# Kernel tuning notes

Measured on AMD Instinct MI355X. Metric: run time of the kernel, lower is better.

## Reference

```python
import jax, jax.numpy as jnp
import numpy as np

D_MODEL = 512
N_HEADS = 8


def setup_inputs() -> dict:
    key = jax.random.key(0)
    ks = jax.random.split(key, 16)
    bs, S, D = 16, 512, D_MODEL
    def lin(k, fo, fi):
        lim = np.sqrt(6.0 / (fi + fo)).astype(np.float32)
        return jax.random.uniform(k, (fo, fi), jnp.float32, -lim, lim)
    inp = {
        'q': jax.random.normal(ks[0], (bs, S, D), jnp.float32),
        'k': jax.random.normal(ks[1], (bs, S, D), jnp.float32),
        'v': jax.random.normal(ks[2], (bs, S, D), jnp.float32),
        'sgap': jax.random.randint(ks[3], (bs, S), 0, 100, jnp.int64) if jax.config.jax_enable_x64 else jax.random.randint(ks[3], (bs, S), 0, 100, jnp.int32),
        'pcount': jax.random.randint(ks[4], (bs, S), 0, 50, jnp.int32),
        'Wq': lin(ks[5], D, D), 'bq': jnp.zeros((D,), jnp.float32),
        'Wk': lin(ks[6], D, D), 'bk': jnp.zeros((D,), jnp.float32),
        'Wv': lin(ks[7], D, D), 'bv': jnp.zeros((D,), jnp.float32),
        'Wo': lin(ks[8], D, D), 'bo': jnp.zeros((D,), jnp.float32),
        'gammas': jax.random.normal(ks[9], (N_HEADS, 1, 1), jnp.float32) * 0.5,
        'ln_g': jnp.ones((D,), jnp.float32), 'ln_b': jnp.zeros((D,), jnp.float32),
        'Wi1': lin(ks[10], D // 4, 2), 'bi1': jnp.zeros((D // 4,), jnp.float32),
        'Wi2': lin(ks[11], D, D // 4), 'bi2': jnp.zeros((D,), jnp.float32),
        'iscale': jnp.array([0.5], jnp.float32),
    }
    return inp


def reference(q, k, v, sgap, pcount, Wq, bq, Wk, bk, Wv, bv, Wo, bo, gammas, ln_g, ln_b, Wi1, bi1, Wi2, bi2, iscale):
    bs, S, D = q.shape
    h = gammas.shape[0]
    d_k = D // h
    def split_heads(x, W, b):
        return (x @ W.T + b).reshape(bs, S, h, d_k).transpose(0, 2, 1, 3)  # [b,h,S,d]
    qh = split_heads(q, Wq, bq)
    kh = split_heads(k, Wk, bk)
    vh = split_heads(v, Wv, bv)

    scores = jnp.einsum('bhid,bhjd->bhij', qh, kh) / jnp.sqrt(jnp.float32(d_k))
    # strict-causal mask (triu(ones,k=0)==0): attend only to j < i
    mask = jnp.tril(jnp.ones((S, S), bool), k=-1)[None, None]
    NEG = jnp.float32(-1e32)

    # no-grad temporal distance term
    p = jax.nn.softmax(jnp.where(mask, scores, NEG), axis=-1) * mask
    distcum = jnp.cumsum(p, axis=-1)
    disttotal = jnp.sum(p, axis=-1, keepdims=True)
    idx = jnp.arange(S, dtype=jnp.float32)
    pos = jnp.abs(idx[None, :] - idx[:, None])[None, None]
    dist = jax.lax.stop_gradient(jnp.sqrt(jnp.clip((disttotal - distcum) * pos, 0.0, None)))

    gam = -jax.nn.softplus(gammas)[None]  # [1,h,1,1]
    temporal = jnp.clip(jnp.exp(dist * gam), 1e-5, 1e5)
    attn = jax.nn.softmax(jnp.where(mask, scores * temporal, NEG), axis=-1)
    attn = attn.at[:, :, 0, :].set(0.0)  # zero_pad first query position

    X = jnp.einsum('bhij,bhjd->bhid', attn, vh).transpose(0, 2, 1, 3).reshape(bs, S, D)

    # InterferenceAddNorm
    def norm01(x):
        x = x.astype(jnp.float32)
        std = jnp.std(x, ddof=1) + 1e-6
        return (jnp.tanh((x - jnp.mean(x)) / std) + 1.0) / 2.0
    ii = jnp.stack([norm01(sgap), norm01(pcount)], axis=-1)  # [b,S,2]
    feat = jax.nn.relu(ii @ Wi1.T + bi1) @ Wi2.T + bi2
    Y = X + iscale * feat
    mu = jnp.mean(Y, -1, keepdims=True)
    var = jnp.var(Y, -1, keepdims=True)
    Yn = (Y - mu) / jnp.sqrt(var + 1e-5) * ln_g + ln_b
    return Yn @ Wo.T + bo
```

## Files before the change

### kernel.cpp

```cpp
#include <hip/hip_runtime.h>
#include <hip/hip_bf16.h>
#include <math.h>

typedef __attribute__((ext_vector_type(8))) short bf16x8;
typedef __attribute__((ext_vector_type(4))) float f32x4;
typedef __fp16 __attribute__((ext_vector_type(2))) h16x2;

__device__ __forceinline__ f32x4 mfma16(bf16x8 a, bf16x8 b, f32x4 c) {
  return __builtin_amdgcn_mfma_f32_16x16x32_bf16(a, b, c, 0, 0, 0);
}

__device__ __forceinline__ float scan16(float x) {
  int v;
  v = __builtin_amdgcn_update_dpp(0, __float_as_int(x), 0x111, 0xf, 0xf, true);
  x += __int_as_float(v);
  v = __builtin_amdgcn_update_dpp(0, __float_as_int(x), 0x112, 0xf, 0xf, true);
  x += __int_as_float(v);
  v = __builtin_amdgcn_update_dpp(0, __float_as_int(x), 0x114, 0xf, 0xf, true);
  x += __int_as_float(v);
  v = __builtin_amdgcn_update_dpp(0, __float_as_int(x), 0x118, 0xf, 0xf, true);
  x += __int_as_float(v);
  return x;
}

__global__ void stats_kernel(const int* __restrict__ sgap,
                             const int* __restrict__ pcount,
                             float* __restrict__ stats) {
  const int N = 16 * 512;
  long long s0 = 0, q0 = 0, s1 = 0, q1 = 0;
  for (int i = threadIdx.x; i < N; i += 256) {
    long long a = sgap[i];
    long long b = pcount[i];
    s0 += a; q0 += a * a;
    s1 += b; q1 += b * b;
  }
#pragma unroll
  for (int m = 32; m >= 1; m >>= 1) {
    s0 += __shfl_xor(s0, m, 64); q0 += __shfl_xor(q0, m, 64);
    s1 += __shfl_xor(s1, m, 64); q1 += __shfl_xor(q1, m, 64);
  }
  __shared__ long long red[4][4];
  const int w = threadIdx.x >> 6;
  if ((threadIdx.x & 63) == 0) {
    red[w][0] = s0; red[w][1] = q0; red[w][2] = s1; red[w][3] = q1;
  }
  __syncthreads();
  if (threadIdx.x == 0) {
    long long S0 = 0, Q0 = 0, S1 = 0, Q1 = 0;
    for (int i = 0; i < 4; ++i) {
      S0 += red[i][0]; Q0 += red[i][1]; S1 += red[i][2]; Q1 += red[i][3];
    }
    const double n = (double)N;
    const double mean0 = S0 / n, mean1 = S1 / n;
    const double var0 = ((double)Q0 - (double)S0 * (double)S0 / n) / (n - 1.0);
    const double var1 = ((double)Q1 - (double)S1 * (double)S1 / n) / (n - 1.0);
    const float std0 = (float)sqrt(var0) + 1e-6f;
    const float std1 = (float)sqrt(var1) + 1e-6f;
    stats[0] = (float)mean0; stats[1] = 1.0f / std0;
    stats[2] = (float)mean1; stats[3] = 1.0f / std1;
  }
}

template <int AMODE>
__device__ __forceinline__ void gemm_body(const void* __restrict__ Ain,
                                          const float* __restrict__ W,
                                          const float* __restrict__ bias,
                                          void* __restrict__ Out, const int omode) {
  constexpr int LDK = 40;
  __shared__ __hip_bfloat16 As[128 * LDK];
  __shared__ __hip_bfloat16 Bs[64 * LDK];
  const int tid = threadIdx.x;
  const int tm = blockIdx.x * 128;
  const int tn = blockIdx.y * 64;
  const int lane = tid & 63;
  const int wid = tid >> 6;
  const int wm = wid * 32;
  const int g = lane >> 4, l15 = lane & 15;

  const f32x4 Z = {0.f, 0.f, 0.f, 0.f};
  f32x4 acc[2][4];
#pragma unroll
  for (int m = 0; m < 2; ++m)
#pragma unroll
    for (int n = 0; n < 4; ++n) acc[m][n] = Z;

  for (int k0 = 0; k0 < 512; k0 += 32) {
#pragma unroll
    for (int p = 0; p < 4; ++p) {
      const int c = p * 256 + tid;
      const int row = c >> 3;
      const int kc = (c & 7) * 4;
      union { __hip_bfloat16 h[4]; uint2 u; } ua;
      if (AMODE == 0) {
        const float4 x = *(const float4*)((const float*)Ain + (size_t)(tm + row) * 512 + k0 + kc);
        ua.h[0] = __float2bfloat16(x.x); ua.h[1] = __float2bfloat16(x.y);
        ua.h[2] = __float2bfloat16(x.z); ua.h[3] = __float2bfloat16(x.w);
      } else {
        ua.u = *(const uint2*)((const __hip_bfloat16*)Ain + (size_t)(tm + row) * 512 + k0 + kc);
      }
      *(uint2*)&As[row * LDK + kc] = ua.u;
      if (p < 2) {
        union { __hip_bfloat16 h[4]; uint2 u; } ub;
        const float4 wv = *(const float4*)(W + (size_t)(tn + row) * 512 + k0 + kc);
        ub.h[0] = __float2bfloat16(wv.x); ub.h[1] = __float2bfloat16(wv.y);
        ub.h[2] = __float2bfloat16(wv.z); ub.h[3] = __float2bfloat16(wv.w);
        *(uint2*)&Bs[row * LDK + kc] = ub.u;
      }
    }
    __syncthreads();
    bf16x8 af[2], bfv[4];
#pragma unroll
    for (int m = 0; m < 2; ++m)
      af[m] = *(const bf16x8*)&As[(wm + m * 16 + l15) * LDK + g * 8];
#pragma unroll
    for (int n = 0; n < 4; ++n)
      bfv[n] = *(const bf16x8*)&Bs[(n * 16 + l15) * LDK + g * 8];
#pragma unroll
    for (int m = 0; m < 2; ++m)
#pragma unroll
      for (int n = 0; n < 4; ++n)
        acc[m][n] = mfma16(af[m], bfv[n], acc[m][n]);
    __syncthreads();
  }

#pragma unroll
  for (int n = 0; n < 4; ++n) {
    const int cc = tn + n * 16 + l15;
    const float bv = bias[cc];
#pragma unroll
    for (int m = 0; m < 2; ++m) {
#pragma unroll
      for (int jj = 0; jj < 4; ++jj) {
        const int r = tm + wm + m * 16 + g * 4 + jj;
        const float v = acc[m][n][jj] + bv;
        if (omode == 2) {
          ((float*)Out)[(size_t)r * 512 + cc] = v;
        } else {
          const int bb = r >> 9, srow = r & 511, hh = cc >> 6, dd = cc & 63;
          if (omode == 0)
            ((__hip_bfloat16*)Out)[(((size_t)(bb * 8 + hh)) * 512 + srow) * 64 + dd] =
                __float2bfloat16(v);
          else
            ((__hip_bfloat16*)Out)[(((size_t)(bb * 8 + hh)) * 64 + dd) * 512 + srow] =
                __float2bfloat16(v);
        }
      }
    }
  }
}

__global__ __launch_bounds__(256) void gemm_qkv(
    const float* __restrict__ q, const float* __restrict__ k,
    const float* __restrict__ v, const float* __restrict__ Wq,
    const float* __restrict__ bq, const float* __restrict__ Wk,
    const float* __restrict__ bk, const float* __restrict__ Wv,
    const float* __restrict__ bv, __hip_bfloat16* __restrict__ qh,
    __hip_bfloat16* __restrict__ kh, __hip_bfloat16* __restrict__ vhT) {
  const int z = blockIdx.z;
  const float* A = (z == 0) ? q : (z == 1) ? k : v;
  const float* W = (z == 0) ? Wq : (z == 1) ? Wk : Wv;
  const float* bias = (z == 0) ? bq : (z == 1) ? bk : bv;
  void* Out = (z == 0) ? (void*)qh : (z == 1) ? (void*)kh : (void*)vhT;
  gemm_body<0>(A, W, bias, Out, (z == 2) ? 1 : 0);
}

__global__ __launch_bounds__(256) void gemm_wo(const __hip_bfloat16* __restrict__ Yn,
                                               const float* __restrict__ Wo,
                                               const float* __restrict__ bo,
                                               float* __restrict__ Out) {
  gemm_body<1>(Yn, Wo, bo, Out, 2);
}

#define PLD 40

__device__ __forceinline__ void attn_unit(
    const __hip_bfloat16* __restrict__ Q, const __hip_bfloat16* __restrict__ K,
    const __hip_bfloat16* __restrict__ V, __hip_bfloat16* __restrict__ Xb,
    __hip_bfloat16* Pw, const int i0, const int ntile, const float gam,
    const int b, const int h, const int lane) {
  const int g = lane >> 4, l15 = lane & 15;
  const float scale = 0.125f;
  const f32x4 Z = {0.f, 0.f, 0.f, 0.f};

  const bf16x8 qf0 = *(const bf16x8*)&Q[(i0 + l15) * 64 + g * 8];
  const bf16x8 qf1 = *(const bf16x8*)&Q[(i0 + l15) * 64 + 32 + g * 8];

  h16x2 sp[64];
  float d1p[4] = {0.f, 0.f, 0.f, 0.f};
#pragma unroll
  for (int t = 0; t < 32; ++t) {
    if (t < ntile) {
      const bf16x8 kf0 = *(const bf16x8*)&K[(t * 16 + l15) * 64 + g * 8];
      const bf16x8 kf1 = *(const bf16x8*)&K[(t * 16 + l15) * 64 + 32 + g * 8];
      f32x4 s = mfma16(qf0, kf0, Z);
      s = mfma16(qf1, kf1, s);
      sp[2 * t] = __builtin_amdgcn_cvt_pkrtz(s[0] * scale, s[1] * scale);
      sp[2 * t + 1] = __builtin_amdgcn_cvt_pkrtz(s[2] * scale, s[3] * scale);
      const int j = t * 16 + l15;
#pragma unroll
      for (int jj = 0; jj < 4; ++jj) {
        const float sv = (float)((jj < 2) ? sp[2 * t][jj] : sp[2 * t + 1][jj - 2]);
        const int i = i0 + g * 4 + jj;
        d1p[jj] += (j < i) ? __expf(sv) : 0.f;
      }
    }
  }
  float invd1[4];
#pragma unroll
  for (int jj = 0; jj < 4; ++jj) {
    float dd = d1p[jj];
#pragma unroll
    for (int m = 8; m >= 1; m >>= 1) dd += __shfl_xor(dd, m, 16);
    invd1[jj] = dd > 0.f ? 1.f / dd : 0.f;
  }

  f32x4 accx[4] = {Z, Z, Z, Z};
  float carry[4] = {0.f, 0.f, 0.f, 0.f};
  float d2p[4] = {0.f, 0.f, 0.f, 0.f};

#pragma unroll
  for (int tp = 0; tp < 16; ++tp) {
    if (tp * 2 < ntile) {
      __hip_bfloat16* Pb = Pw + (tp & 1) * (16 * PLD);
#pragma unroll
      for (int half = 0; half < 2; ++half) {
        const int t = tp * 2 + half;
        float e2v[4] = {0.f, 0.f, 0.f, 0.f};
        if (t < ntile) {
          const int j = t * 16 + l15;
#pragma unroll
          for (int jj = 0; jj < 4; ++jj) {
            const float sv = (float)((jj < 2) ? sp[2 * t][jj] : sp[2 * t + 1][jj - 2]);
            const int i = i0 + g * 4 + jj;
            const bool valid = j < i;
            const float p = valid ? __expf(sv) * invd1[jj] : 0.f;
            const float cs = scan16(p) + carry[jj];
            const float suffix = 1.f - cs;
            carry[jj] = __shfl(cs, 15, 16);
            const float dist = sqrtf(fmaxf(suffix * (float)(i - j), 0.f));
            const float tempo = fmaxf(__expf(gam * dist), 1e-5f);
            const float e2 = valid ? __expf(sv * tempo) : 0.f;
            d2p[jj] += e2;
            e2v[jj] = e2;
          }
        }
#pragma unroll
        for (int jj = 0; jj < 4; ++jj)
          Pb[(g * 4 + jj) * PLD + half * 16 + l15] = __float2bfloat16(e2v[jj]);
      }
      asm volatile("s_waitcnt lgkmcnt(0)" ::: "memory");
      const bf16x8 pf = *(const bf16x8*)&Pb[l15 * PLD + g * 8];
#pragma unroll
      for (int n = 0; n < 4; ++n) {
        const bf16x8 vf =
            *(const bf16x8*)&V[(size_t)(n * 16 + l15) * 512 + tp * 32 + g * 8];
        accx[n] = mfma16(pf, vf, accx[n]);
      }
    }
  }

#pragma unroll
  for (int jj = 0; jj < 4; ++jj) {
    float dd = d2p[jj];
#pragma unroll
    for (int m = 8; m >= 1; m >>= 1) dd += __shfl_xor(dd, m, 16);
    d2p[jj] = dd > 0.f ? 1.f / dd : 0.f;
  }
#pragma unroll
  for (int n = 0; n < 4; ++n) {
#pragma unroll
    for (int jj = 0; jj < 4; ++jj) {
      const int i = i0 + g * 4 + jj;
      const float val = (i > 0) ? accx[n][jj] * d2p[jj] : 0.f;
      Xb[((size_t)(b * 512 + i)) * 512 + h * 64 + n * 16 + l15] = __float2bfloat16(val);
    }
  }
}

__global__ __launch_bounds__(64, 4) void attn_kernel(
    const __hip_bfloat16* __restrict__ qh, const __hip_bfloat16* __restrict__ kh,
    const __hip_bfloat16* __restrict__ vhT, const float* __restrict__ gammas,
    __hip_bfloat16* __restrict__ Xb) {
  __shared__ __hip_bfloat16 Psh[2 * 16 * PLD];
  const int lane = threadIdx.x;
  const int work = (blockIdx.x & 7) * 512 + (blockIdx.x >> 3);
  const int bh = work >> 5;
  const int rg = work & 31;
  const int b = bh >> 3, h = bh & 7;

  const __hip_bfloat16* Q = qh + (size_t)bh * (512 * 64);
  const __hip_bfloat16* K = kh + (size_t)bh * (512 * 64);
  const __hip_bfloat16* V = vhT + (size_t)bh * (64 * 512);
  const float gam = -log1pf(expf(gammas[h]));

  attn_unit(Q, K, V, Xb, Psh, rg * 16, rg + 1, gam, b, h, lane);
}

__global__ __launch_bounds__(256) void addnorm_kernel(
    const __hip_bfloat16* __restrict__ Xb, const int* __restrict__ sgap,
    const int* __restrict__ pcount, const float* __restrict__ stats,
    const float* __restrict__ Wi1, const float* __restrict__ bi1,
    const float* __restrict__ Wi2, const float* __restrict__ bi2,
    const float* __restrict__ iscale, const float* __restrict__ ln_g,
    const float* __restrict__ ln_b, __hip_bfloat16* __restrict__ Yn) {
  constexpr int WLD = 132;
  __shared__ __hip_bfloat16 Hs[16 * WLD];
  __shared__ float iis[16][2];
  __shared__ float red[4][16][2];
  const int tid = threadIdx.x;
  const int lane = tid & 63;
  const int w = tid >> 6;
  const int g = lane >> 4, l15 = lane & 15;
  const int t0 = blockIdx.x * 16;

  if (tid < 16) {
    const float a0 = ((float)sgap[t0 + tid] - stats[0]) * stats[1];
    const float a1 = ((float)pcount[t0 + tid] - stats[2]) * stats[3];
    iis[tid][0] = (tanhf(a0) + 1.f) * 0.5f;
    iis[tid][1] = (tanhf(a1) + 1.f) * 0.5f;
  }
  __syncthreads();

  {
    const int tt = tid & 15;
    const int jb = (tid >> 4) * 8;
    const float a = iis[tt][0], b = iis[tt][1];
#pragma unroll
    for (int jj = 0; jj < 8; ++jj) {
      const int j = jb + jj;
      const float hv = fmaxf(Wi1[j * 2] * a + Wi1[j * 2 + 1] * b + bi1[j], 0.f);
      Hs[tt * WLD + j] = __float2bfloat16(hv);
    }
  }
  __syncthreads();

  const f32x4 Z = {0.f, 0.f, 0.f, 0.f};
  f32x4 acc[8];
#pragma unroll
  for (int n = 0; n < 8; ++n) acc[n] = Z;

#pragma unroll
  for (int k = 0; k < 4; ++k) {
    const bf16x8 af = *(const bf16x8*)&Hs[l15 * WLD + k * 32 + g * 8];
#pragma unroll
    for (int n = 0; n < 8; ++n) {
      const int col = w * 128 + n * 16 + l15;
      const float4 x0 = *(const float4*)(Wi2 + (size_t)col * 128 + k * 32 + g * 8);
      const float4 x1 = *(const float4*)(Wi2 + (size_t)col * 128 + k * 32 + g * 8 + 4);
      union { __hip_bfloat16 hh[8]; bf16x8 v8; } ub;
      ub.hh[0] = __float2bfloat16(x0.x); ub.hh[1] = __float2bfloat16(x0.y);
      ub.hh[2] = __float2bfloat16(x0.z); ub.hh[3] = __float2bfloat16(x0.w);
      ub.hh[4] = __float2bfloat16(x1.x); ub.hh[5] = __float2bfloat16(x1.y);
      ub.hh[6] = __float2bfloat16(x1.z); ub.hh[7] = __float2bfloat16(x1.w);
      acc[n] = mfma16(af, ub.v8, acc[n]);
    }
  }

  const float sc = iscale[0];
  float bi[8], lg[8], lb[8];
#pragma unroll
  for (int nn = 0; nn < 8; ++nn) {
    const int c = w * 128 + nn * 16 + l15;
    bi[nn] = bi2[c]; lg[nn] = ln_g[c]; lb[nn] = ln_b[c];
  }

#pragma unroll
  for (int jj = 0; jj < 4; ++jj) {
    const int r = g * 4 + jj;
    float s = 0.f, sq = 0.f;
#pragma unroll
    for (int nn = 0; nn < 8; ++nn) {
      const int c = w * 128 + nn * 16 + l15;
      const float fv = acc[nn][jj] + bi[nn];
      const float y = __bfloat162float(Xb[(size_t)(t0 + r) * 512 + c]) + sc * fv;
      acc[nn][jj] = y;
      s += y; sq += y * y;
    }
#pragma unroll
    for (int mk = 8; mk >= 1; mk >>= 1) {
      s += __shfl_xor(s, mk, 16);
      sq += __shfl_xor(sq, mk, 16);
    }
    if (l15 == 0) { red[w][r][0] = s; red[w][r][1] = sq; }
  }
  __syncthreads();

#pragma unroll
  for (int jj = 0; jj < 4; ++jj) {
    const int r = g * 4 + jj;
    const float sum = red[0][r][0] + red[1][r][0] + red[2][r][0] + red[3][r][0];
    const float sqs = red[0][r][1] + red[1][r][1] + red[2][r][1] + red[3][r][1];
    const float mu = sum * (1.f / 512.f);
    const float var = sqs * (1.f / 512.f) - mu * mu;
    const float rstd = rsqrtf(var + 1e-5f);
#pragma unroll
    for (int nn = 0; nn < 8; ++nn) {
      const int c = w * 128 + nn * 16 + l15;
      Yn[(size_t)(t0 + r) * 512 + c] =
          __float2bfloat16((acc[nn][jj] - mu) * rstd * lg[nn] + lb[nn]);
    }
  }
}

extern "C" void kernel_launch(void* const* d_in, const int* in_sizes, int n_in,
                              void* d_out, int out_size, void* d_ws, size_t ws_size,
                              hipStream_t stream) {
  const float* q = (const float*)d_in[0];
  const float* k = (const float*)d_in[1];
  const float* v = (const float*)d_in[2];
  const int* sgap = (const int*)d_in[3];
  const int* pcount = (const int*)d_in[4];
  const float* Wq = (const float*)d_in[5];
  const float* bq = (const float*)d_in[6];
  const float* Wk = (const float*)d_in[7];
  const float* bk = (const float*)d_in[8];
  const float* Wv = (const float*)d_in[9];
  const float* bv = (const float*)d_in[10];
  const float* Wo = (const float*)d_in[11];
  const float* bo = (const float*)d_in[12];
  const float* gammas = (const float*)d_in[13];
  const float* ln_g = (const float*)d_in[14];
  const float* ln_b = (const float*)d_in[15];
  const float* Wi1 = (const float*)d_in[16];
  const float* bi1 = (const float*)d_in[17];
  const float* Wi2 = (const float*)d_in[18];
  const float* bi2 = (const float*)d_in[19];
  const float* iscale = (const float*)d_in[20];

  char* ws = (char*)d_ws;
  __hip_bfloat16* qh = (__hip_bfloat16*)(ws);
  __hip_bfloat16* kh = (__hip_bfloat16*)(ws + ((size_t)8 << 20));
  __hip_bfloat16* vhT = (__hip_bfloat16*)(ws + ((size_t)16 << 20));
  __hip_bfloat16* Xb = (__hip_bfloat16*)(ws + ((size_t)24 << 20));
  __hip_bfloat16* Yn = (__hip_bfloat16*)(ws + ((size_t)32 << 20));
  float* stats = (float*)(ws + ((size_t)40 << 20));

  stats_kernel<<<1, 256, 0, stream>>>(sgap, pcount, stats);
  gemm_qkv<<<dim3(64, 8, 3), 256, 0, stream>>>(q, k, v, Wq, bq, Wk, bk, Wv, bv,
                                               qh, kh, vhT);
  attn_kernel<<<4096, 64, 0, stream>>>(qh, kh, vhT, gammas, Xb);
  addnorm_kernel<<<512, 256, 0, stream>>>(Xb, sgap, pcount, stats, Wi1, bi1, Wi2,
                                          bi2, iscale, ln_g, ln_b, Yn);
  gemm_wo<<<dim3(64, 8), 256, 0, stream>>>(Yn, Wo, bo, (float*)d_out);
}
```

Before: 293.4 us.

## Pre-convert weights to bf16, enlarge GEMM tiles to 128x128, remap blocks for locality

Adds a small kernel that converts Wq/Wk/Wv/Wo to bf16 once per call, so the GEMMs load bf16 weight tiles directly with 16-byte loads instead of converting fp32 in each block. The GEMM tile grows from 128x64 to 128x128, with each of four waves computing a 64x64 subtile, which raises reuse of A per block and halves the block count. Block indices are remapped with an XCD-style interleave to improve L2 locality across chiplets. The attention kernel's occupancy hint is dropped. The cost is an extra kernel launch and more accumulator registers per wave, which can reduce GEMM occupancy.

New measurement: 279.6 us. 4.7% less time.

```diff
diff --git a/kernel.cpp b/kernel.cpp
--- a/kernel.cpp
+++ b/kernel.cpp
@@ -61,26 +61,41 @@
   }
 }
 
+__global__ __launch_bounds__(256) void cvtW_kernel(
+    const float* __restrict__ Wq, const float* __restrict__ Wk,
+    const float* __restrict__ Wv, const float* __restrict__ Wo,
+    __hip_bfloat16* __restrict__ Wbf) {
+  const int i = blockIdx.x * 256 + threadIdx.x;
+  const int sel = i >> 16;
+  const int off = i & 65535;
+  const float* W = (sel == 0) ? Wq : (sel == 1) ? Wk : (sel == 2) ? Wv : Wo;
+  const float4 x = *(const float4*)(W + (size_t)off * 4);
+  union { __hip_bfloat16 h[4]; uint2 u; } ub;
+  ub.h[0] = __float2bfloat16(x.x); ub.h[1] = __float2bfloat16(x.y);
+  ub.h[2] = __float2bfloat16(x.z); ub.h[3] = __float2bfloat16(x.w);
+  *(uint2*)(Wbf + (size_t)i * 4) = ub.u;
+}
+
 template <int AMODE>
 __device__ __forceinline__ void gemm_body(const void* __restrict__ Ain,
-                                          const float* __restrict__ W,
+                                          const __hip_bfloat16* __restrict__ Wb,
                                           const float* __restrict__ bias,
-                                          void* __restrict__ Out, const int omode) {
+                                          void* __restrict__ Out, const int omode,
+                                          const int tm, const int tn) {
   constexpr int LDK = 40;
   __shared__ __hip_bfloat16 As[128 * LDK];
-  __shared__ __hip_bfloat16 Bs[64 * LDK];
+  __shared__ __hip_bfloat16 Bs[128 * LDK];
   const int tid = threadIdx.x;
-  const int tm = blockIdx.x * 128;
-  const int tn = blockIdx.y * 64;
   const int lane = tid & 63;
   const int wid = tid >> 6;
-  const int wm = wid * 32;
+  const int wm = (wid >> 1) * 64;
+  const int wn = (wid & 1) * 64;
   const int g = lane >> 4, l15 = lane & 15;
 
   const f32x4 Z = {0.f, 0.f, 0.f, 0.f};
-  f32x4 acc[2][4];
-#pragma unroll
-  for (int m = 0; m < 2; ++m)
+  f32x4 acc[4][4];
+#pragma unroll
+  for (int m = 0; m < 4; ++m)
 #pragma unroll
     for (int n = 0; n < 4; ++n) acc[m][n] = Z;
 
@@ -99,24 +114,25 @@
         ua.u = *(const uint2*)((const __hip_bfloat16*)Ain + (size_t)(tm + row) * 512 + k0 + kc);
       }
       *(uint2*)&As[row * LDK + kc] = ua.u;
-      if (p < 2) {
-        union { __hip_bfloat16 h[4]; uint2 u; } ub;
-        const float4 wv = *(const float4*)(W + (size_t)(tn + row) * 512 + k0 + kc);
-        ub.h[0] = __float2bfloat16(wv.x); ub.h[1] = __float2bfloat16(wv.y);
-        ub.h[2] = __float2bfloat16(wv.z); ub.h[3] = __float2bfloat16(wv.w);
-        *(uint2*)&Bs[row * LDK + kc] = ub.u;
-      }
+    }
+#pragma unroll
+    for (int p = 0; p < 2; ++p) {
+      const int c = p * 256 + tid;
+      const int row = c >> 2;
+      const int kc = (c & 3) * 8;
+      *(uint4*)&Bs[row * LDK + kc] =
+          *(const uint4*)(Wb + (size_t)(tn + row) * 512 + k0 + kc);
     }
     __syncthreads();
-    bf16x8 af[2], bfv[4];
-#pragma unroll
-    for (int m = 0; m < 2; ++m)
+    bf16x8 af[4], bfv[4];
+#pragma unroll
+    for (int m = 0; m < 4; ++m)
       af[m] = *(const bf16x8*)&As[(wm + m * 16 + l15) * LDK + g * 8];
 #pragma unroll
     for (int n = 0; n < 4; ++n)
-      bfv[n] = *(const bf16x8*)&Bs[(n * 16 + l15) * LDK + g * 8];
-#pragma unroll
-    for (int m = 0; m < 2; ++m)
+      bfv[n] = *(const bf16x8*)&Bs[(wn + n * 16 + l15) * LDK + g * 8];
+#pragma unroll
+    for (int m = 0; m < 4; ++m)
 #pragma unroll
       for (int n = 0; n < 4; ++n)
         acc[m][n] = mfma16(af[m], bfv[n], acc[m][n]);
@@ -125,10 +141,10 @@
 
 #pragma unroll
   for (int n = 0; n < 4; ++n) {
-    const int cc = tn + n * 16 + l15;
+    const int cc = tn + wn + n * 16 + l15;
     const float bv = bias[cc];
 #pragma unroll
-    for (int m = 0; m < 2; ++m) {
+    for (int m = 0; m < 4; ++m) {
 #pragma unroll
       for (int jj = 0; jj < 4; ++jj) {
         const int r = tm + wm + m * 16 + g * 4 + jj;
@@ -151,24 +167,31 @@
 
 __global__ __launch_bounds__(256) void gemm_qkv(
     const float* __restrict__ q, const float* __restrict__ k,
-    const float* __restrict__ v, const float* __restrict__ Wq,
-    const float* __restrict__ bq, const float* __restrict__ Wk,
-    const float* __restrict__ bk, const float* __restrict__ Wv,
-    const float* __restrict__ bv, __hip_bfloat16* __restrict__ qh,
+    const float* __restrict__ v, const float* __restrict__ bq,
+    const float* __restrict__ bk, const float* __restrict__ bv,
+    const __hip_bfloat16* __restrict__ Wbf, __hip_bfloat16* __restrict__ qh,
     __hip_bfloat16* __restrict__ kh, __hip_bfloat16* __restrict__ vhT) {
-  const int z = blockIdx.z;
+  const int flat = blockIdx.x + 4 * blockIdx.y + 256 * blockIdx.z;
+  const int L = (flat & 7) * 96 + (flat >> 3);
+  const int z = L >> 8;
+  const int rem = L & 255;
+  const int tm = (rem >> 2) * 128;
+  const int tn = (rem & 3) * 128;
   const float* A = (z == 0) ? q : (z == 1) ? k : v;
-  const float* W = (z == 0) ? Wq : (z == 1) ? Wk : Wv;
   const float* bias = (z == 0) ? bq : (z == 1) ? bk : bv;
   void* Out = (z == 0) ? (void*)qh : (z == 1) ? (void*)kh : (void*)vhT;
-  gemm_body<0>(A, W, bias, Out, (z == 2) ? 1 : 0);
+  gemm_body<0>(A, Wbf + (size_t)z * (512 * 512), bias, Out, (z == 2) ? 1 : 0, tm, tn);
 }
 
 __global__ __launch_bounds__(256) void gemm_wo(const __hip_bfloat16* __restrict__ Yn,
-                                               const float* __restrict__ Wo,
+                                               const __hip_bfloat16* __restrict__ Wbf,
                                                const float* __restrict__ bo,
                                                float* __restrict__ Out) {
-  gemm_body<1>(Yn, Wo, bo, Out, 2);
+  const int flat = blockIdx.x + 4 * blockIdx.y;
+  const int L = (flat & 7) * 32 + (flat >> 3);
+  const int tm = (L >> 2) * 128;
+  const int tn = (L & 3) * 128;
+  gemm_body<1>(Yn, Wbf + (size_t)3 * (512 * 512), bo, Out, 2, tm, tn);
 }
 
 #define PLD 40
@@ -277,7 +300,7 @@
   }
 }
 
-__global__ __launch_bounds__(64, 4) void attn_kernel(
+__global__ __launch_bounds__(64) void attn_kernel(
     const __hip_bfloat16* __restrict__ qh, const __hip_bfloat16* __restrict__ kh,
     const __hip_bfloat16* __restrict__ vhT, const float* __restrict__ gammas,
     __hip_bfloat16* __restrict__ Xb) {
@@ -433,13 +456,15 @@
   __hip_bfloat16* vhT = (__hip_bfloat16*)(ws + ((size_t)16 << 20));
   __hip_bfloat16* Xb = (__hip_bfloat16*)(ws + ((size_t)24 << 20));
   __hip_bfloat16* Yn = (__hip_bfloat16*)(ws + ((size_t)32 << 20));
-  float* stats = (float*)(ws + ((size_t)40 << 20));
+  __hip_bfloat16* Wbf = (__hip_bfloat16*)(ws + ((size_t)40 << 20));
+  float* stats = (float*)(ws + ((size_t)42 << 20));
 
   stats_kernel<<<1, 256, 0, stream>>>(sgap, pcount, stats);
-  gemm_qkv<<<dim3(64, 8, 3), 256, 0, stream>>>(q, k, v, Wq, bq, Wk, bk, Wv, bv,
+  cvtW_kernel<<<1024, 256, 0, stream>>>(Wq, Wk, Wv, Wo, Wbf);
+  gemm_qkv<<<dim3(4, 64, 3), 256, 0, stream>>>(q, k, v, bq, bk, bv, Wbf,
                                                qh, kh, vhT);
   attn_kernel<<<4096, 64, 0, stream>>>(qh, kh, vhT, gammas, Xb);
   addnorm_kernel<<<512, 256, 0, stream>>>(Xb, sgap, pcount, stats, Wi1, bi1, Wi2,
                                           bi2, iscale, ln_g, ln_b, Yn);
-  gemm_wo<<<dim3(64, 8), 256, 0, stream>>>(Yn, Wo, bo, (float*)d_out);
-}
+  gemm_wo<<<dim3(4, 64), 256, 0, stream>>>(Yn, Wbf, bo, (float*)d_out);
+}
```
